# Kernel tuning notes

Hardware: AMD Instinct MI355X
Metric: run time of the kernel (lower is better)

## Reference

```python
import jax, jax.numpy as jnp
import numpy as np

D_MODEL = 1024
N_HEADS = 16
D_HEAD = D_MODEL // N_HEADS


def setup_inputs() -> dict:
    key = jax.random.key(0)
    k1, k2, k3 = jax.random.split(key, 3)
    x = jax.random.normal(k1, (2, 2048, D_MODEL), dtype=jnp.float32)
    # Dense layer params (glorot-ish scale)
    W_qkv = jax.random.normal(k2, (D_MODEL, 3 * D_MODEL), dtype=jnp.float32) * (1.0 / np.sqrt(D_MODEL))
    b_qkv = jnp.zeros((3 * D_MODEL,), dtype=jnp.float32)
    W_proj = jax.random.normal(k3, (D_MODEL, D_MODEL), dtype=jnp.float32) * (1.0 / np.sqrt(D_MODEL))
    b_proj = jnp.zeros((D_MODEL,), dtype=jnp.float32)
    return {"x": x, "W_qkv": W_qkv, "b_qkv": b_qkv, "W_proj": W_proj, "b_proj": b_proj}


def reference(x, W_qkv, b_qkv, W_proj, b_proj):
    B, S, _ = x.shape
    qkv = x @ W_qkv + b_qkv                      # [B,S,3D]
    q, k, v = jnp.split(qkv, 3, axis=-1)
    # [B,S,D] -> [B,H,S,Dh]
    def to_heads(t):
        return t.reshape(B, S, N_HEADS, D_HEAD).transpose(0, 2, 1, 3)
    q, k, v = to_heads(q), to_heads(k), to_heads(v)
    scores = jnp.einsum('bhqd,bhkd->bhqk', q, k)  # [B,H,S,S]
    causal = jnp.tril(jnp.ones((S, S), dtype=bool))
    # NOTE: mask applied BEFORE scaling, matching the original module.
    scores = jnp.where(causal[None, None, :, :], scores, jnp.float32(-1e9))
    scaled = scores / jnp.sqrt(jnp.float32(D_HEAD))
    attn = jax.nn.softmax(scaled, axis=-1)
    ctx = jnp.einsum('bhqk,bhkd->bhqd', attn, v)  # [B,H,S,Dh]
    ctx = ctx.transpose(0, 2, 1, 3).reshape(B, S, D_MODEL)
    return ctx @ W_proj + b_proj
```

## Files before the change

### kernel.cpp

```cpp
#include <hip/hip_runtime.h>
#include <stdint.h>

typedef __attribute__((ext_vector_type(8))) short short8;
typedef __attribute__((ext_vector_type(4))) float f32x4;

__device__ __forceinline__ unsigned short f2b(float f) {
  union { float f; uint32_t u; } v; v.f = f;
  uint32_t u = v.u;
  u = u + 0x7fffu + ((u >> 16) & 1u);
  return (unsigned short)(u >> 16);
}
__device__ __forceinline__ float b2f(unsigned short s) {
  union { uint32_t u; float f; } v; v.u = ((uint32_t)s) << 16;
  return v.f;
}
__device__ __forceinline__ unsigned int cvtpk(float lo, float hi) {
  unsigned int r;
  asm("v_cvt_pk_bf16_f32 %0, %1, %2" : "=v"(r) : "v"(lo), "v"(hi));
  return r;
}
__device__ __forceinline__ void gload16(const void* g, void* lds) {
  __builtin_amdgcn_global_load_lds((const __attribute__((address_space(1))) void*)g,
                                   (__attribute__((address_space(3))) void*)lds, 16, 0, 0);
}

__global__ __launch_bounds__(256) void cvt_f32_bf16(const float* __restrict__ in,
                                                    unsigned short* __restrict__ out, int n) {
  int i = (blockIdx.x * 256 + threadIdx.x) * 4;
  if (i < n) {
    float4 v = *(const float4*)(in + i);
    ushort4 o;
    o.x = f2b(v.x); o.y = f2b(v.y); o.z = f2b(v.z); o.w = f2b(v.w);
    *(ushort4*)(out + i) = o;
  }
}

__global__ __launch_bounds__(256) void transposeW(const float* __restrict__ W,
                                                  unsigned short* __restrict__ Wt,
                                                  int K, int N) {
  __shared__ float tile[32][33];
  int x0 = blockIdx.x * 32, y0 = blockIdx.y * 32;
  int tx = threadIdx.x, ty = threadIdx.y;
  #pragma unroll
  for (int j = 0; j < 4; ++j)
    tile[ty + j * 8][tx] = W[(size_t)(y0 + ty + j * 8) * N + x0 + tx];
  __syncthreads();
  #pragma unroll
  for (int j = 0; j < 4; ++j)
    Wt[(size_t)(x0 + ty + j * 8) * K + y0 + tx] = f2b(tile[tx][ty + j * 8]);
}

template<bool OUTF32>
__global__ __launch_bounds__(256) void gemm_bt(const unsigned short* __restrict__ A,
                                               const unsigned short* __restrict__ Bt,
                                               const float* __restrict__ bias,
                                               void* __restrict__ outp,
                                               int M, int N, int K) {
  __shared__ unsigned short As[128 * 32];
  __shared__ unsigned short Bs[128 * 32];
  const int t = threadIdx.x;
  const int lane = t & 63;
  const int w = t >> 6;
  const int wm = w >> 1, wn = w & 1;
  const int m0 = blockIdx.x * 128, n0 = blockIdx.y * 128;
  const f32x4 zero = {0.f, 0.f, 0.f, 0.f};
  f32x4 acc[4][4];
  #pragma unroll
  for (int i = 0; i < 4; ++i)
    #pragma unroll
    for (int j = 0; j < 4; ++j) acc[i][j] = zero;

  const int srow = t >> 2;
  const int sc   = t & 3;

  for (int k0 = 0; k0 < K; k0 += 32) {
    __syncthreads();
    #pragma unroll
    for (int hh = 0; hh < 2; ++hh) {
      gload16(A  + (size_t)(m0 + hh * 64 + srow) * K + k0 + sc * 8,
              (char*)As + hh * 4096 + w * 1024);
      gload16(Bt + (size_t)(n0 + hh * 64 + srow) * K + k0 + sc * 8,
              (char*)Bs + hh * 4096 + w * 1024);
    }
    __syncthreads();
    short8 af[4], bfr[4];
    #pragma unroll
    for (int f = 0; f < 4; ++f) {
      af[f]  = *(const short8*)(As + (wm * 64 + f * 16 + (lane & 15)) * 32 + (lane >> 4) * 8);
      bfr[f] = *(const short8*)(Bs + (wn * 64 + f * 16 + (lane & 15)) * 32 + (lane >> 4) * 8);
    }
    #pragma unroll
    for (int fm = 0; fm < 4; ++fm)
      #pragma unroll
      for (int fn = 0; fn < 4; ++fn)
        acc[fm][fn] = __builtin_amdgcn_mfma_f32_16x16x32_bf16(af[fm], bfr[fn], acc[fm][fn], 0, 0, 0);
  }

  const int cl = lane & 15, g = lane >> 4;
  #pragma unroll
  for (int fn = 0; fn < 4; ++fn) {
    int col = n0 + wn * 64 + fn * 16 + cl;
    float bv = bias[col];
    #pragma unroll
    for (int fm = 0; fm < 4; ++fm) {
      int rbase = m0 + wm * 64 + fm * 16 + g * 4;
      #pragma unroll
      for (int r = 0; r < 4; ++r) {
        float vout = acc[fm][fn][r] + bv;
        if (OUTF32) ((float*)outp)[(size_t)(rbase + r) * N + col] = vout;
        else ((unsigned short*)outp)[(size_t)(rbase + r) * N + col] = f2b(vout);
      }
    }
  }
}

__global__ __launch_bounds__(256) void transposeV(const unsigned short* __restrict__ qkv,
                                                  unsigned short* __restrict__ Vt) {
  __shared__ unsigned short tile[64][72];
  const int bh = blockIdx.y, b = bh >> 4, h = bh & 15;
  const int s0 = blockIdx.x * 64;
  const int t = threadIdx.x;
  #pragma unroll
  for (int i = 0; i < 2; ++i) {
    int c = t + i * 256;
    int srow = c >> 3, d0 = (c & 7) * 8;
    short8 v = *(const short8*)(qkv + (size_t)(b * 2048 + s0 + srow) * 3072 + 2048 + h * 64 + d0);
    *(short8*)(&tile[srow][d0]) = v;
  }
  __syncthreads();
  #pragma unroll
  for (int i = 0; i < 2; ++i) {
    int c = t + i * 256;
    int d = c >> 3, sb = (c & 7) * 8;
    short8 o;
    #pragma unroll
    for (int j = 0; j < 8; ++j) o[j] = tile[sb + j][d];
    *(short8*)(Vt + (size_t)(bh * 64 + d) * 2048 + s0 + sb) = o;
  }
}

#define ZSCALE 0.18033688011112043f

__device__ __forceinline__ void qkt_phase(const short8 ak[4][2], const short8 bq[2],
                                          char* Pbuf, f32x4 o[4], float& m, float& l,
                                          bool maskIter, int cl, int g, int w) {
  f32x4 st[4];
  #pragma unroll
  for (int tt = 0; tt < 4; ++tt) st[tt] = (f32x4){0.f, 0.f, 0.f, 0.f};
  #pragma unroll
  for (int kk = 0; kk < 2; ++kk)
    #pragma unroll
    for (int tt = 0; tt < 4; ++tt)
      st[tt] = __builtin_amdgcn_mfma_f32_16x16x32_bf16(ak[tt][kk], bq[kk], st[tt], 0, 0, 0);

  float z[4][4];
  #pragma unroll
  for (int tt = 0; tt < 4; ++tt)
    #pragma unroll
    for (int r = 0; r < 4; ++r) z[tt][r] = st[tt][r] * ZSCALE;
  if (maskIter) {
    int q_loc = w * 16 + cl;
    #pragma unroll
    for (int tt = 0; tt < 4; ++tt)
      #pragma unroll
      for (int r = 0; r < 4; ++r)
        if (tt * 16 + 4 * g + r > q_loc) z[tt][r] = -1e30f;
  }
  float v = z[0][0];
  #pragma unroll
  for (int tt = 0; tt < 4; ++tt)
    #pragma unroll
    for (int r = 0; r < 4; ++r) v = fmaxf(v, z[tt][r]);
  v = fmaxf(v, __shfl_xor(v, 16));
  v = fmaxf(v, __shfl_xor(v, 32));
  float mn = fmaxf(m, v);
  float alpha = exp2f(m - mn);
  m = mn;
  float ps = 0.f;
  unsigned int pb[4][2];
  #pragma unroll
  for (int tt = 0; tt < 4; ++tt) {
    float p0 = exp2f(z[tt][0] - m), p1 = exp2f(z[tt][1] - m);
    float p2 = exp2f(z[tt][2] - m), p3 = exp2f(z[tt][3] - m);
    ps += (p0 + p1) + (p2 + p3);
    pb[tt][0] = cvtpk(p0, p1);
    pb[tt][1] = cvtpk(p2, p3);
  }
  ps += __shfl_xor(ps, 16);
  ps += __shfl_xor(ps, 32);
  l = l * alpha + ps;
  #pragma unroll
  for (int c = 0; c < 4; ++c)
    #pragma unroll
    for (int r = 0; r < 4; ++r) o[c][r] *= alpha;

  #pragma unroll
  for (int tt = 0; tt < 4; ++tt) {
    uint2 val; val.x = pb[tt][0]; val.y = pb[tt][1];
    *(uint2*)(Pbuf + ((cl * 128 + tt * 32 + g * 8) ^ ((cl & 7) << 4))) = val;
  }
}

__device__ __forceinline__ void pv_phase(const short8 av[4][2], const char* Pbuf,
                                         f32x4 o[4], int cl, int g) {
  short8 bp[2];
  #pragma unroll
  for (int kk = 0; kk < 2; ++kk)
    bp[kk] = *(const short8*)(Pbuf + ((cl * 128 + kk * 64 + g * 16) ^ ((cl & 7) << 4)));
  #pragma unroll
  for (int kk = 0; kk < 2; ++kk)
    #pragma unroll
    for (int c = 0; c < 4; ++c)
      o[c] = __builtin_amdgcn_mfma_f32_16x16x32_bf16(av[c][kk], bp[kk], o[c], 0, 0, 0);
}

__global__ __launch_bounds__(256, 2) void attn_mfma2(const unsigned short* __restrict__ qkv,
                                                     const unsigned short* __restrict__ Vt,
                                                     unsigned short* __restrict__ ctx) {
  const int p  = blockIdx.x;
  const int bh = blockIdx.y;
  const int b = bh >> 4, h = bh & 15;
  const int qtA = p, qtB = 31 - p;
  const int t = threadIdx.x;
  const int l = t & 63;
  const int w = t >> 6;
  const int cl = l & 15;
  const int g  = l >> 4;

  __shared__ unsigned short Ks[64 * 64];
  __shared__ unsigned short Vs[64 * 64];
  __shared__ unsigned short Ps[4][2][16 * 64];

  char* KsB = (char*)Ks;
  char* VsB = (char*)Vs;
  char* PbA = (char*)(&Ps[w][0][0]);
  char* PbB = (char*)(&Ps[w][1][0]);

  const size_t kbase  = (size_t)(b * 2048) * 3072 + 1024 + h * 64;
  const size_t vtbase = (size_t)(bh * 64) * 2048;

  short8 bqA[2], bqB[2];
  {
    const unsigned short* qa = qkv + (size_t)(b * 2048 + qtA * 64 + w * 16 + cl) * 3072 + h * 64 + g * 8;
    bqA[0] = *(const short8*)(qa);
    bqA[1] = *(const short8*)(qa + 32);
    const unsigned short* qb = qkv + (size_t)(b * 2048 + qtB * 64 + w * 16 + cl) * 3072 + h * 64 + g * 8;
    bqB[0] = *(const short8*)(qb);
    bqB[1] = *(const short8*)(qb + 32);
  }

  f32x4 oA[4], oB[4];
  #pragma unroll
  for (int c = 0; c < 4; ++c) { oA[c] = (f32x4){0.f,0.f,0.f,0.f}; oB[c] = (f32x4){0.f,0.f,0.f,0.f}; }
  float mA = -1e30f, lA = 0.f, mB = -1e30f, lB = 0.f;

  for (int jt = 0; jt <= qtB; ++jt) {
    __syncthreads();
    #pragma unroll
    for (int i = 0; i < 2; ++i) {
      int row = i * 32 + w * 8 + (l >> 3);
      int ch  = (l & 7) ^ (l >> 3);
      gload16(qkv + kbase + (size_t)(jt * 64 + row) * 3072 + ch * 8,
              KsB + i * 4096 + w * 1024);
      gload16(Vt + vtbase + (size_t)row * 2048 + jt * 64 + ch * 8,
              VsB + i * 4096 + w * 1024);
    }
    __syncthreads();

    short8 ak[4][2];
    #pragma unroll
    for (int tt = 0; tt < 4; ++tt)
      #pragma unroll
      for (int kk = 0; kk < 2; ++kk)
        ak[tt][kk] = *(const short8*)(KsB + (((tt * 16 + cl) * 128 + kk * 64 + g * 16) ^ ((cl & 7) << 4)));

    bool actA = (jt <= qtA);
    if (actA) qkt_phase(ak, bqA, PbA, oA, mA, lA, jt == qtA, cl, g, w);
    qkt_phase(ak, bqB, PbB, oB, mB, lB, jt == qtB, cl, g, w);

    short8 av[4][2];
    #pragma unroll
    for (int c = 0; c < 4; ++c)
      #pragma unroll
      for (int kk = 0; kk < 2; ++kk)
        av[c][kk] = *(const short8*)(VsB + (((c * 16 + cl) * 128 + kk * 64 + g * 16) ^ ((cl & 7) << 4)));

    if (actA) pv_phase(av, PbA, oA, cl, g);
    pv_phase(av, PbB, oB, cl, g);
  }

  {
    float inv = 1.f / lA;
    unsigned short* crow = ctx + (size_t)(b * 2048 + qtA * 64 + w * 16 + cl) * 1024 + h * 64 + g * 4;
    #pragma unroll
    for (int c = 0; c < 4; ++c) {
      uint2 val;
      val.x = cvtpk(oA[c][0] * inv, oA[c][1] * inv);
      val.y = cvtpk(oA[c][2] * inv, oA[c][3] * inv);
      *(uint2*)(crow + c * 16) = val;
    }
  }
  {
    float inv = 1.f / lB;
    unsigned short* crow = ctx + (size_t)(b * 2048 + qtB * 64 + w * 16 + cl) * 1024 + h * 64 + g * 4;
    #pragma unroll
    for (int c = 0; c < 4; ++c) {
      uint2 val;
      val.x = cvtpk(oB[c][0] * inv, oB[c][1] * inv);
      val.y = cvtpk(oB[c][2] * inv, oB[c][3] * inv);
      *(uint2*)(crow + c * 16) = val;
    }
  }
}

extern "C" void kernel_launch(void* const* d_in, const int* in_sizes, int n_in,
                              void* d_out, int out_size, void* d_ws, size_t ws_size,
                              hipStream_t stream) {
  const float* x     = (const float*)d_in[0];
  const float* Wqkv  = (const float*)d_in[1];
  const float* bqkv  = (const float*)d_in[2];
  const float* Wproj = (const float*)d_in[3];
  const float* bproj = (const float*)d_in[4];
  float* out = (float*)d_out;

  char* ws = (char*)d_ws;
  unsigned short* xb     = (unsigned short*)(ws);
  unsigned short* wqkvT  = (unsigned short*)(ws + 8388608);
  unsigned short* wprojT = (unsigned short*)(ws + 14680064);
  unsigned short* qkv    = (unsigned short*)(ws + 16777216);
  unsigned short* ctx    = (unsigned short*)(ws + 41943040);
  unsigned short* vt     = (unsigned short*)(ws + 50331648);

  cvt_f32_bf16<<<4096, 256, 0, stream>>>(x, xb, 4096 * 1024);

  dim3 tb(32, 8);
  transposeW<<<dim3(3072 / 32, 1024 / 32), tb, 0, stream>>>(Wqkv, wqkvT, 1024, 3072);
  transposeW<<<dim3(1024 / 32, 1024 / 32), tb, 0, stream>>>(Wproj, wprojT, 1024, 1024);

  gemm_bt<false><<<dim3(32, 24), 256, 0, stream>>>(xb, wqkvT, bqkv, qkv, 4096, 3072, 1024);

  transposeV<<<dim3(32, 32), 256, 0, stream>>>(qkv, vt);

  attn_mfma2<<<dim3(16, 32), 256, 0, stream>>>(qkv, vt, ctx);

  gemm_bt<true><<<dim3(32, 8), 256, 0, stream>>>(ctx, wprojT, bproj, out, 4096, 1024, 1024);
}
```

Baseline: 215.2 us.

## Fold softmax scale into Q weights, lazy rescale, MFMA row-sum, deeper GEMM K-tile

Folds the softmax scale into the Q columns of W_qkv and b_qkv, so the attention kernel no longer multiplies each score. Online softmax now skips the rescale of the accumulators unless the running max grows by more than 8 in log2 units. The row sum is computed by an extra MFMA against a ones tile rather than by shuffles. The GEMM moves to a K-tile of 64 with an XOR-swizzled LDS layout, a block-index swizzle for cache locality, and s_setprio around the MFMA sections. Folding the scale into bf16 Q changes rounding slightly, and the lazy rescale depends on the threshold staying within fp32 range.

Result: no change. 212.5 us (-1.2%).

```diff
diff --git a/kernel.cpp b/kernel.cpp
--- a/kernel.cpp
+++ b/kernel.cpp
@@ -3,16 +3,14 @@
 
 typedef __attribute__((ext_vector_type(8))) short short8;
 typedef __attribute__((ext_vector_type(4))) float f32x4;
+
+#define QSCALE 0.18033688011112043f
 
 __device__ __forceinline__ unsigned short f2b(float f) {
   union { float f; uint32_t u; } v; v.f = f;
   uint32_t u = v.u;
   u = u + 0x7fffu + ((u >> 16) & 1u);
   return (unsigned short)(u >> 16);
-}
-__device__ __forceinline__ float b2f(unsigned short s) {
-  union { uint32_t u; float f; } v; v.u = ((uint32_t)s) << 16;
-  return v.f;
 }
 __device__ __forceinline__ unsigned int cvtpk(float lo, float hi) {
   unsigned int r;
@@ -37,7 +35,7 @@
 
 __global__ __launch_bounds__(256) void transposeW(const float* __restrict__ W,
                                                   unsigned short* __restrict__ Wt,
-                                                  int K, int N) {
+                                                  int K, int N, float scale, int scaleRows) {
   __shared__ float tile[32][33];
   int x0 = blockIdx.x * 32, y0 = blockIdx.y * 32;
   int tx = threadIdx.x, ty = threadIdx.y;
@@ -46,8 +44,11 @@
     tile[ty + j * 8][tx] = W[(size_t)(y0 + ty + j * 8) * N + x0 + tx];
   __syncthreads();
   #pragma unroll
-  for (int j = 0; j < 4; ++j)
-    Wt[(size_t)(x0 + ty + j * 8) * K + y0 + tx] = f2b(tile[tx][ty + j * 8]);
+  for (int j = 0; j < 4; ++j) {
+    int orow = x0 + ty + j * 8;
+    float s = (orow < scaleRows) ? scale : 1.0f;
+    Wt[(size_t)orow * K + y0 + tx] = f2b(tile[tx][ty + j * 8] * s);
+  }
 }
 
 template<bool OUTF32>
@@ -55,14 +56,20 @@
                                                const unsigned short* __restrict__ Bt,
                                                const float* __restrict__ bias,
                                                void* __restrict__ outp,
-                                               int M, int N, int K) {
-  __shared__ unsigned short As[128 * 32];
-  __shared__ unsigned short Bs[128 * 32];
+                                               int M, int N, int K,
+                                               float bscale, int bscaleN, int mtiles) {
+  __shared__ unsigned short As[128 * 64];
+  __shared__ unsigned short Bs[128 * 64];
   const int t = threadIdx.x;
   const int lane = t & 63;
   const int w = t >> 6;
   const int wm = w >> 1, wn = w & 1;
-  const int m0 = blockIdx.x * 128, n0 = blockIdx.y * 128;
+
+  const int cpx = gridDim.x >> 3;
+  const int swz = (blockIdx.x & 7) * cpx + (blockIdx.x >> 3);
+  const int m0 = (swz % mtiles) * 128;
+  const int n0 = (swz / mtiles) * 128;
+
   const f32x4 zero = {0.f, 0.f, 0.f, 0.f};
   f32x4 acc[4][4];
   #pragma unroll
@@ -70,37 +77,46 @@
     #pragma unroll
     for (int j = 0; j < 4; ++j) acc[i][j] = zero;
 
-  const int srow = t >> 2;
-  const int sc   = t & 3;
-
-  for (int k0 = 0; k0 < K; k0 += 32) {
+  const int cl = lane & 15, g = lane >> 4;
+  const int srow = t >> 3;
+  const int sch  = (t & 7) ^ (srow & 7);
+
+  char* AsB = (char*)As;
+  char* BsB = (char*)Bs;
+
+  for (int k0 = 0; k0 < K; k0 += 64) {
     __syncthreads();
     #pragma unroll
-    for (int hh = 0; hh < 2; ++hh) {
-      gload16(A  + (size_t)(m0 + hh * 64 + srow) * K + k0 + sc * 8,
-              (char*)As + hh * 4096 + w * 1024);
-      gload16(Bt + (size_t)(n0 + hh * 64 + srow) * K + k0 + sc * 8,
-              (char*)Bs + hh * 4096 + w * 1024);
+    for (int r = 0; r < 4; ++r) {
+      int row = r * 32 + srow;
+      gload16(A  + (size_t)(m0 + row) * K + k0 + sch * 8, AsB + r * 4096 + t * 16);
+      gload16(Bt + (size_t)(n0 + row) * K + k0 + sch * 8, BsB + r * 4096 + t * 16);
     }
     __syncthreads();
-    short8 af[4], bfr[4];
-    #pragma unroll
-    for (int f = 0; f < 4; ++f) {
-      af[f]  = *(const short8*)(As + (wm * 64 + f * 16 + (lane & 15)) * 32 + (lane >> 4) * 8);
-      bfr[f] = *(const short8*)(Bs + (wn * 64 + f * 16 + (lane & 15)) * 32 + (lane >> 4) * 8);
-    }
-    #pragma unroll
-    for (int fm = 0; fm < 4; ++fm)
-      #pragma unroll
-      for (int fn = 0; fn < 4; ++fn)
-        acc[fm][fn] = __builtin_amdgcn_mfma_f32_16x16x32_bf16(af[fm], bfr[fn], acc[fm][fn], 0, 0, 0);
-  }
-
-  const int cl = lane & 15, g = lane >> 4;
+    #pragma unroll
+    for (int kk = 0; kk < 2; ++kk) {
+      short8 af[4], bfr[4];
+      #pragma unroll
+      for (int f = 0; f < 4; ++f) {
+        int arow = wm * 64 + f * 16 + cl;
+        int brow = wn * 64 + f * 16 + cl;
+        af[f]  = *(const short8*)(AsB + ((arow * 128 + kk * 64 + g * 16) ^ ((cl & 7) << 4)));
+        bfr[f] = *(const short8*)(BsB + ((brow * 128 + kk * 64 + g * 16) ^ ((cl & 7) << 4)));
+      }
+      __builtin_amdgcn_s_setprio(1);
+      #pragma unroll
+      for (int fm = 0; fm < 4; ++fm)
+        #pragma unroll
+        for (int fn = 0; fn < 4; ++fn)
+          acc[fm][fn] = __builtin_amdgcn_mfma_f32_16x16x32_bf16(af[fm], bfr[fn], acc[fm][fn], 0, 0, 0);
+      __builtin_amdgcn_s_setprio(0);
+    }
+  }
+
   #pragma unroll
   for (int fn = 0; fn < 4; ++fn) {
     int col = n0 + wn * 64 + fn * 16 + cl;
-    float bv = bias[col];
+    float bv = bias[col] * ((col < bscaleN) ? bscale : 1.0f);
     #pragma unroll
     for (int fm = 0; fm < 4; ++fm) {
       int rbase = m0 + wm * 64 + fm * 16 + g * 4;
@@ -139,25 +155,26 @@
   }
 }
 
-#define ZSCALE 0.18033688011112043f
-
-__device__ __forceinline__ void qkt_phase(const short8 ak[4][2], const short8 bq[2],
-                                          char* Pbuf, f32x4 o[4], float& m, float& l,
-                                          bool maskIter, int cl, int g, int w) {
+__device__ __forceinline__ void attn_tile(const short8 ak[4][2], const short8 av[4][2],
+                                          const short8 a5[2], const short8 bq[2],
+                                          char* Pbuf, f32x4 o[4], f32x4& o5,
+                                          float& m, bool maskIter, int cl, int g, int w) {
   f32x4 st[4];
   #pragma unroll
   for (int tt = 0; tt < 4; ++tt) st[tt] = (f32x4){0.f, 0.f, 0.f, 0.f};
+  __builtin_amdgcn_s_setprio(1);
   #pragma unroll
   for (int kk = 0; kk < 2; ++kk)
     #pragma unroll
     for (int tt = 0; tt < 4; ++tt)
       st[tt] = __builtin_amdgcn_mfma_f32_16x16x32_bf16(ak[tt][kk], bq[kk], st[tt], 0, 0, 0);
+  __builtin_amdgcn_s_setprio(0);
 
   float z[4][4];
   #pragma unroll
   for (int tt = 0; tt < 4; ++tt)
     #pragma unroll
-    for (int r = 0; r < 4; ++r) z[tt][r] = st[tt][r] * ZSCALE;
+    for (int r = 0; r < 4; ++r) z[tt][r] = st[tt][r];
   if (maskIter) {
     int q_loc = w * 16 + cl;
     #pragma unroll
@@ -166,52 +183,48 @@
       for (int r = 0; r < 4; ++r)
         if (tt * 16 + 4 * g + r > q_loc) z[tt][r] = -1e30f;
   }
-  float v = z[0][0];
+  float cm = z[0][0];
   #pragma unroll
   for (int tt = 0; tt < 4; ++tt)
     #pragma unroll
-    for (int r = 0; r < 4; ++r) v = fmaxf(v, z[tt][r]);
-  v = fmaxf(v, __shfl_xor(v, 16));
-  v = fmaxf(v, __shfl_xor(v, 32));
-  float mn = fmaxf(m, v);
-  float alpha = exp2f(m - mn);
-  m = mn;
-  float ps = 0.f;
-  unsigned int pb[4][2];
+    for (int r = 0; r < 4; ++r) cm = fmaxf(cm, z[tt][r]);
+  cm = fmaxf(cm, __shfl_xor(cm, 16));
+  cm = fmaxf(cm, __shfl_xor(cm, 32));
+
+  if (!__all(cm <= m + 8.f)) {
+    float mn = fmaxf(m, cm);
+    float alpha = exp2f(m - mn);
+    m = mn;
+    #pragma unroll
+    for (int c = 0; c < 4; ++c)
+      #pragma unroll
+      for (int r = 0; r < 4; ++r) o[c][r] *= alpha;
+    o5[0] *= alpha;
+  }
+
   #pragma unroll
   for (int tt = 0; tt < 4; ++tt) {
     float p0 = exp2f(z[tt][0] - m), p1 = exp2f(z[tt][1] - m);
     float p2 = exp2f(z[tt][2] - m), p3 = exp2f(z[tt][3] - m);
-    ps += (p0 + p1) + (p2 + p3);
-    pb[tt][0] = cvtpk(p0, p1);
-    pb[tt][1] = cvtpk(p2, p3);
-  }
-  ps += __shfl_xor(ps, 16);
-  ps += __shfl_xor(ps, 32);
-  l = l * alpha + ps;
-  #pragma unroll
-  for (int c = 0; c < 4; ++c)
-    #pragma unroll
-    for (int r = 0; r < 4; ++r) o[c][r] *= alpha;
-
-  #pragma unroll
-  for (int tt = 0; tt < 4; ++tt) {
-    uint2 val; val.x = pb[tt][0]; val.y = pb[tt][1];
+    uint2 val;
+    val.x = cvtpk(p0, p1);
+    val.y = cvtpk(p2, p3);
     *(uint2*)(Pbuf + ((cl * 128 + tt * 32 + g * 8) ^ ((cl & 7) << 4))) = val;
   }
-}
-
-__device__ __forceinline__ void pv_phase(const short8 av[4][2], const char* Pbuf,
-                                         f32x4 o[4], int cl, int g) {
   short8 bp[2];
   #pragma unroll
   for (int kk = 0; kk < 2; ++kk)
     bp[kk] = *(const short8*)(Pbuf + ((cl * 128 + kk * 64 + g * 16) ^ ((cl & 7) << 4)));
-  #pragma unroll
-  for (int kk = 0; kk < 2; ++kk)
+
+  __builtin_amdgcn_s_setprio(1);
+  #pragma unroll
+  for (int kk = 0; kk < 2; ++kk) {
     #pragma unroll
     for (int c = 0; c < 4; ++c)
       o[c] = __builtin_amdgcn_mfma_f32_16x16x32_bf16(av[c][kk], bp[kk], o[c], 0, 0, 0);
+    o5 = __builtin_amdgcn_mfma_f32_16x16x32_bf16(a5[kk], bp[kk], o5, 0, 0, 0);
+  }
+  __builtin_amdgcn_s_setprio(0);
 }
 
 __global__ __launch_bounds__(256, 2) void attn_mfma2(const unsigned short* __restrict__ qkv,
@@ -230,11 +243,26 @@
   __shared__ unsigned short Ks[64 * 64];
   __shared__ unsigned short Vs[64 * 64];
   __shared__ unsigned short Ps[4][2][16 * 64];
+  __shared__ unsigned short Ones[16 * 64];
 
   char* KsB = (char*)Ks;
   char* VsB = (char*)Vs;
   char* PbA = (char*)(&Ps[w][0][0]);
   char* PbB = (char*)(&Ps[w][1][0]);
+  char* OnB = (char*)Ones;
+
+  {
+    int row = t >> 4;
+    int c4  = (t & 15) * 4;
+    unsigned short vv = (row == 0) ? (unsigned short)0x3F80 : (unsigned short)0;
+    ushort4 ov = {vv, vv, vv, vv};
+    *(ushort4*)(OnB + ((row * 128 + c4 * 2) ^ ((row & 7) << 4))) = ov;
+  }
+  __syncthreads();
+  short8 a5[2];
+  #pragma unroll
+  for (int kk = 0; kk < 2; ++kk)
+    a5[kk] = *(const short8*)(OnB + ((cl * 128 + kk * 64 + g * 16) ^ ((cl & 7) << 4)));
 
   const size_t kbase  = (size_t)(b * 2048) * 3072 + 1024 + h * 64;
   const size_t vtbase = (size_t)(bh * 64) * 2048;
@@ -249,10 +277,12 @@
     bqB[1] = *(const short8*)(qb + 32);
   }
 
-  f32x4 oA[4], oB[4];
+  f32x4 oA[4], oB[4], o5A, o5B;
   #pragma unroll
   for (int c = 0; c < 4; ++c) { oA[c] = (f32x4){0.f,0.f,0.f,0.f}; oB[c] = (f32x4){0.f,0.f,0.f,0.f}; }
-  float mA = -1e30f, lA = 0.f, mB = -1e30f, lB = 0.f;
+  o5A = (f32x4){0.f,0.f,0.f,0.f};
+  o5B = (f32x4){0.f,0.f,0.f,0.f};
+  float mA = -1e30f, mB = -1e30f;
 
   for (int jt = 0; jt <= qtB; ++jt) {
     __syncthreads();
@@ -273,11 +303,6 @@
       #pragma unroll
       for (int kk = 0; kk < 2; ++kk)
         ak[tt][kk] = *(const short8*)(KsB + (((tt * 16 + cl) * 128 + kk * 64 + g * 16) ^ ((cl & 7) << 4)));
-
-    bool actA = (jt <= qtA);
-    if (actA) qkt_phase(ak, bqA, PbA, oA, mA, lA, jt == qtA, cl, g, w);
-    qkt_phase(ak, bqB, PbB, oB, mB, lB, jt == qtB, cl, g, w);
-
     short8 av[4][2];
     #pragma unroll
     for (int c = 0; c < 4; ++c)
@@ -285,12 +310,13 @@
       for (int kk = 0; kk < 2; ++kk)
         av[c][kk] = *(const short8*)(VsB + (((c * 16 + cl) * 128 + kk * 64 + g * 16) ^ ((cl & 7) << 4)));
 
-    if (actA) pv_phase(av, PbA, oA, cl, g);
-    pv_phase(av, PbB, oB, cl, g);
+    if (jt <= qtA) attn_tile(ak, av, a5, bqA, PbA, oA, o5A, mA, jt == qtA, cl, g, w);
+    attn_tile(ak, av, a5, bqB, PbB, oB, o5B, mB, jt == qtB, cl, g, w);
   }
 
   {
-    float inv = 1.f / lA;
+    float lsum = __shfl(o5A[0], cl);
+    float inv = 1.f / lsum;
     unsigned short* crow = ctx + (size_t)(b * 2048 + qtA * 64 + w * 16 + cl) * 1024 + h * 64 + g * 4;
     #pragma unroll
     for (int c = 0; c < 4; ++c) {
@@ -301,7 +327,8 @@
     }
   }
   {
-    float inv = 1.f / lB;
+    float lsum = __shfl(o5B[0], cl);
+    float inv = 1.f / lsum;
     unsigned short* crow = ctx + (size_t)(b * 2048 + qtB * 64 + w * 16 + cl) * 1024 + h * 64 + g * 4;
     #pragma unroll
     for (int c = 0; c < 4; ++c) {
@@ -334,14 +361,16 @@
   cvt_f32_bf16<<<4096, 256, 0, stream>>>(x, xb, 4096 * 1024);
 
   dim3 tb(32, 8);
-  transposeW<<<dim3(3072 / 32, 1024 / 32), tb, 0, stream>>>(Wqkv, wqkvT, 1024, 3072);
-  transposeW<<<dim3(1024 / 32, 1024 / 32), tb, 0, stream>>>(Wproj, wprojT, 1024, 1024);
-
-  gemm_bt<false><<<dim3(32, 24), 256, 0, stream>>>(xb, wqkvT, bqkv, qkv, 4096, 3072, 1024);
+  transposeW<<<dim3(3072 / 32, 1024 / 32), tb, 0, stream>>>(Wqkv, wqkvT, 1024, 3072, QSCALE, 1024);
+  transposeW<<<dim3(1024 / 32, 1024 / 32), tb, 0, stream>>>(Wproj, wprojT, 1024, 1024, 1.0f, 0);
+
+  gemm_bt<false><<<768, 256, 0, stream>>>(xb, wqkvT, bqkv, qkv, 4096, 3072, 1024,
+                                          QSCALE, 1024, 32);
 
   transposeV<<<dim3(32, 32), 256, 0, stream>>>(qkv, vt);
 
   attn_mfma2<<<dim3(16, 32), 256, 0, stream>>>(qkv, vt, ctx);
 
-  gemm_bt<true><<<dim3(32, 8), 256, 0, stream>>>(ctx, wprojT, bproj, out, 4096, 1024, 1024);
-}
+  gemm_bt<true><<<256, 256, 0, stream>>>(ctx, wprojT, bproj, out, 4096, 1024, 1024,
+                                         1.0f, 0, 32);
+}
```
